# Performance work log

Measured on AMD Instinct MI355X. Metric: run time of the kernel, lower is better.

Reference implementation:

```python
import jax, jax.numpy as jnp
import numpy as np

NEG_INF = -1e9  # 'close_to_negative_inf' constant from the original code


def setup_inputs() -> dict:
    B, S, H, DH, W = 4, 2048, 16, 64, 4
    D = H * DH
    KC = (S - W) // W + 1  # compressed k/v length (VALID conv, stride=W)
    key = jax.random.key(0)
    ks = jax.random.split(key, 9)
    return {
        "pre_q": jax.random.normal(ks[0], (B, S, H, DH), jnp.float32),
        "pre_v": jax.random.normal(ks[1], (B, S, H, DH), jnp.float32),
        "pre_k": jax.random.normal(ks[2], (B, S, H, DH), jnp.float32),
        "output_weights": jax.random.normal(ks[3], (D, D), jnp.float32) * (1.0 / np.sqrt(D)),
        "k_conv_kernel": jax.random.normal(ks[4], (W, DH, DH), jnp.float32) * (1.0 / np.sqrt(W * DH)),
        "k_conv_bias": jnp.zeros((DH,), jnp.float32),
        "v_conv_kernel": jax.random.normal(ks[5], (W, DH, DH), jnp.float32) * (1.0 / np.sqrt(W * DH)),
        "v_conv_bias": jnp.zeros((DH,), jnp.float32),
        "attn_mask": jax.random.randint(ks[6], (B, S, KC), 0, 2, jnp.int32),
    }


def _compress(x, kernel, bias, window):
    # x: (B, H, S, dh) -> conv1d channels_last, stride=window, VALID -> (B, H, Kc, dh)
    B, H, S, dh = x.shape
    x3 = x.reshape(B * H, S, dh)
    y = jax.lax.conv_general_dilated(
        x3, kernel, window_strides=(window,), padding='VALID',
        dimension_numbers=('NWC', 'WIO', 'NWC')) + bias
    return y.reshape(B, H, -1, dh)


def reference(pre_q, pre_v, pre_k, output_weights,
              k_conv_kernel, k_conv_bias, v_conv_kernel, v_conv_bias,
              attn_mask):
    B, Sq, H, dh = pre_q.shape
    d_model = H * dh
    window = k_conv_kernel.shape[0]

    q = jnp.transpose(pre_q, (0, 2, 1, 3))  # (B,H,Sq,dh)
    v = jnp.transpose(pre_v, (0, 2, 1, 3))
    k = jnp.transpose(pre_k, (0, 2, 1, 3))

    # memory-compressed attention: strided conv1d over k and v sequences
    k = _compress(k, k_conv_kernel, k_conv_bias, window)  # (B,H,Kc,dh)
    v = _compress(v, v_conv_kernel, v_conv_bias, window)  # (B,H,Kc,dh)
    Kc = k.shape[2]

    sqrt_d = jnp.sqrt(jnp.float32(d_model // H))

    # batch_dot over merged (B*H) batch dim, exactly as the Keras code
    scores = jnp.matmul(q.reshape(B * H, Sq, dh),
                        jnp.transpose(k, (0, 1, 3, 2)).reshape(B * H, dh, Kc)) / sqrt_d

    # mask_attention: reshape (B*H,q,k) -> (H,B,q,k), apply mask, permute back (faithful to original)
    s4 = scores.reshape(H, B, Sq, Kc)
    m = attn_mask.astype(jnp.float32)  # (B,Sq,Kc), broadcasts over heads
    s4 = s4 * m + (1.0 - m) * NEG_INF
    scores = jnp.transpose(s4, (1, 0, 2, 3)).reshape(B * H, Sq, Kc)

    probs = jax.nn.softmax(scores, axis=-1)  # dropout=0.0 -> identity

    heads = jnp.matmul(probs, v.reshape(B * H, Kc, dh)).reshape(B, H, Sq, dh)
    merged = jnp.transpose(heads, (0, 2, 1, 3)).reshape(-1, d_model)  # (B*Sq, D)
    out = jnp.dot(merged, output_weights).reshape(B, Sq, d_model)
    return out
```

## Files before the change

### kernel.cpp

```cpp
#include <hip/hip_runtime.h>
#include <hip/hip_bf16.h>


typedef __attribute__((ext_vector_type(8))) short short8;
typedef __attribute__((ext_vector_type(4))) short short4v;
typedef __attribute__((ext_vector_type(4))) float f32x4;
typedef __attribute__((ext_vector_type(4))) int int4e;
typedef __attribute__((ext_vector_type(2))) unsigned int u32x2;

#define MFMA32(A, Bf, C) __builtin_amdgcn_mfma_f32_16x16x32_bf16((A), (Bf), (C), 0, 0, 0)
#define MFMA16(A, Bf, C) __builtin_amdgcn_mfma_f32_16x16x16bf16_1k((A), (Bf), (C), 0, 0, 0)

static __device__ __forceinline__ unsigned short f2bf(float f) {
  unsigned int u = __builtin_bit_cast(unsigned int, f);
  u += 0x7fffu + ((u >> 16) & 1u);
  return (unsigned short)(u >> 16);
}
static __device__ __forceinline__ unsigned int pack2c(float a, float b) {
  unsigned short lo = __builtin_bit_cast(unsigned short, __float2bfloat16(a));
  unsigned short hi = __builtin_bit_cast(unsigned short, __float2bfloat16(b));
  return (unsigned int)lo | ((unsigned int)hi << 16);
}
static __device__ __forceinline__ short4v pk4(float a, float b, float c, float d) {
  u32x2 t;
  t[0] = pack2c(a, b);
  t[1] = pack2c(c, d);
  return __builtin_bit_cast(short4v, t);
}
static __device__ __forceinline__ short8 cvt8(f32x4 lo, f32x4 hi) {
  short8 r;
  r[0] = (short)f2bf(lo[0]); r[1] = (short)f2bf(lo[1]);
  r[2] = (short)f2bf(lo[2]); r[3] = (short)f2bf(lo[3]);
  r[4] = (short)f2bf(hi[0]); r[5] = (short)f2bf(hi[1]);
  r[6] = (short)f2bf(hi[2]); r[7] = (short)f2bf(hi[3]);
  return r;
}
static __device__ __forceinline__ short8 cvt8s(f32x4 lo, f32x4 hi, float s) {
  short8 r;
  r[0] = (short)f2bf(lo[0]*s); r[1] = (short)f2bf(lo[1]*s);
  r[2] = (short)f2bf(lo[2]*s); r[3] = (short)f2bf(lo[3]*s);
  r[4] = (short)f2bf(hi[0]*s); r[5] = (short)f2bf(hi[1]*s);
  r[6] = (short)f2bf(hi[2]*s); r[7] = (short)f2bf(hi[3]*s);
  return r;
}
static __device__ __forceinline__ void gl_lds16(const void* g, void* l) {
  __builtin_amdgcn_global_load_lds(
      (const __attribute__((address_space(1))) unsigned int*)g,
      (__attribute__((address_space(3))) unsigned int*)l, 16, 0, 0);
}

__global__ __launch_bounds__(256) void prep_kernel(
    const float* __restrict__ W, unsigned short* __restrict__ WT,
    const float* __restrict__ kck, unsigned short* __restrict__ kkT,
    const float* __restrict__ vck, unsigned short* __restrict__ vkT,
    const int* __restrict__ msk, unsigned int* __restrict__ mpk) {
  __shared__ unsigned short t[64][72];
  const int bid = blockIdx.x;
  const int tid = threadIdx.x;
  if (bid < 256) {
    const int k0 = (bid & 15) * 64, n0 = (bid >> 4) * 64;
    const int cr = tid >> 4, cc = (tid & 15) * 4;
    #pragma unroll
    for (int it = 0; it < 4; ++it) {
      const int kk = it * 16 + cr;
      const f32x4 v = *(const f32x4*)(W + (size_t)(k0 + kk) * 1024 + n0 + cc);
      #pragma unroll
      for (int j = 0; j < 4; ++j) t[cc + j][kk] = f2bf(v[j]);
    }
    __syncthreads();
    const int rn = tid >> 2, seg = tid & 3;
    const short8 w0 = *(const short8*)(&t[rn][seg * 16]);
    const short8 w1 = *(const short8*)(&t[rn][seg * 16 + 8]);
    unsigned short* op = WT + (size_t)(n0 + rn) * 1024 + k0 + seg * 16;
    *(short8*)op = w0;
    *(short8*)(op + 8) = w1;
  } else if (bid < 384) {
    const int tb = bid - 256;
    const float* K = (tb < 64) ? kck : vck;
    unsigned short* KT = (tb < 64) ? kkT : vkT;
    const int idx = (tb & 63) * 256 + tid;
    const int kk = idx >> 6, o = idx & 63;
    KT[o * 256 + kk] = f2bf(K[idx]);
  } else {
    const int w = (bid - 384) * 256 + tid;
    const int* p = msk + (size_t)w * 32;
    unsigned int b = 0;
    #pragma unroll
    for (int i = 0; i < 8; ++i) {
      const int4e v = *(const int4e*)(p + i * 4);
      b |= (unsigned int)(v[0] & 1) << (i * 4);
      b |= (unsigned int)(v[1] & 1) << (i * 4 + 1);
      b |= (unsigned int)(v[2] & 1) << (i * 4 + 2);
      b |= (unsigned int)(v[3] & 1) << (i * 4 + 3);
    }
    mpk[w] = b;
  }
}

__global__ __launch_bounds__(256) void compress_kernel(
    const float* __restrict__ srcK, const unsigned short* __restrict__ kTK,
    const float* __restrict__ biasK, unsigned short* __restrict__ dstK,
    const float* __restrict__ srcV, const unsigned short* __restrict__ kTV,
    const float* __restrict__ biasV, unsigned short* __restrict__ dstV) {
  __shared__ unsigned short t[64 * 72];
  const int bid = blockIdx.x;
  const int tpose = bid >> 9;
  const float* src = tpose ? srcV : srcK;
  const unsigned short* kT = tpose ? kTV : kTK;
  const float* bias = tpose ? biasV : biasK;
  unsigned short* dst = tpose ? dstV : dstK;
  const int tid = threadIdx.x;
  const int wid = tid >> 6, lane = tid & 63;
  const int q = lane & 15, g = lane >> 4;
  const int blockR0 = (bid & 511) * 64;
  const int R0 = blockR0 + wid * 16;
  const int row = R0 + q;
  const int bh = row >> 9, c = row & 511;
  const int b = bh >> 4, h = bh & 15;
  const float* sb = src + (((size_t)b * 2048 + (size_t)c * 4) * 16 + h) * 64;
  f32x4 acc[4];
  #pragma unroll
  for (int ct = 0; ct < 4; ++ct) acc[ct] = f32x4{0.f, 0.f, 0.f, 0.f};
  #pragma unroll
  for (int ch = 0; ch < 8; ++ch) {
    const int kk = ch * 32 + g * 8;
    const int w = kk >> 6, i = kk & 63;
    const float* s8 = sb + (size_t)w * 1024 + i;
    short8 a = cvt8(*(const f32x4*)s8, *(const f32x4*)(s8 + 4));
    #pragma unroll
    for (int ct = 0; ct < 4; ++ct) {
      short8 bf = *(const short8*)(kT + (ct * 16 + q) * 256 + ch * 32 + g * 8);
      acc[ct] = MFMA32(a, bf, acc[ct]);
    }
  }
  #pragma unroll
  for (int ct = 0; ct < 4; ++ct) {
    const int col = ct * 16 + q;
    const float bv = bias[col];
    #pragma unroll
    for (int r = 0; r < 4; ++r) {
      const int lr = wid * 16 + 4 * g + r;
      const unsigned short val = f2bf(acc[ct][r] + bv);
      t[tpose ? (col * 72 + lr) : (lr * 72 + col)] = val;
    }
  }
  __syncthreads();
  const int d = tid >> 2, sq = tid & 3;
  const short8 w0 = *(const short8*)(&t[d * 72 + sq * 16]);
  const short8 w1 = *(const short8*)(&t[d * 72 + sq * 16 + 8]);
  unsigned short* op;
  if (tpose) {
    const int bhb = blockR0 >> 9, cb = blockR0 & 511;
    op = dst + (size_t)bhb * 32768 + (size_t)d * 512 + cb + sq * 16;
  } else {
    op = dst + (size_t)(blockR0 + d) * 64 + sq * 16;
  }
  *(short8*)op = w0;
  *(short8*)(op + 8) = w1;
}

__global__ __launch_bounds__(256) void attn_kernel(
    const float* __restrict__ preq, const unsigned int* __restrict__ mpk,
    const unsigned short* __restrict__ kc, const unsigned short* __restrict__ vt,
    unsigned short* __restrict__ merged) {
  __shared__ unsigned short shm[9728];
  unsigned short* Kl = shm;
  unsigned short* Vl = shm + 4608;
  const int tid = threadIdx.x;
  const int wid = tid >> 6, lane = tid & 63;
  const int q = lane & 15, g = lane >> 4;
  const int bid = blockIdx.x;
  const int x = bid & 7, ii = bid >> 3;
  const int bp = x >> 1;
  const int hp = ((x & 1) << 3) | (ii & 7);
  const int tile = ii >> 3;
  const int jj = hp * 4 + bp;
  const int bin = jj >> 4, hin = jj & 15;
  const int s0 = tile * 128 + wid * 32;

  const float QS = 0.18033688f;
  const float* qpA = preq + (((size_t)bin * 2048 + s0 + q) * 16 + hin) * 64;
  const float* qpB = qpA + 16 * 1024;
  const short8 bqA0 = cvt8s(*(const f32x4*)(qpA + g * 8), *(const f32x4*)(qpA + g * 8 + 4), QS);
  const short8 bqA1 = cvt8s(*(const f32x4*)(qpA + 32 + g * 8), *(const f32x4*)(qpA + 32 + g * 8 + 4), QS);
  const short8 bqB0 = cvt8s(*(const f32x4*)(qpB + g * 8), *(const f32x4*)(qpB + g * 8 + 4), QS);
  const short8 bqB1 = cvt8s(*(const f32x4*)(qpB + 32 + g * 8), *(const f32x4*)(qpB + 32 + g * 8 + 4), QS);

  const unsigned short* kcb = kc + (size_t)jj * 512 * 64;
  const unsigned short* vtb = vt + (size_t)(bp * 16 + hp) * 64 * 512;
  const unsigned int* mrowA = mpk + ((size_t)bp * 2048 + s0 + q) * 16;
  const unsigned int* mrowB = mrowA + 256;

  const int krow = tid >> 3, kc8 = tid & 7;
  const unsigned short* gK = kcb + (size_t)krow * 64 + kc8 * 8;
  unsigned short* lK = Kl + krow * 72 + kc8 * 8;
  const int vrow = tid >> 2, vc4 = tid & 3;
  const unsigned short* gV = vtb + (size_t)vrow * 512 + vc4 * 8;
  unsigned short* lV = Vl + vrow * 40 + vc4 * 8;

  const short4v one4 = {(short)0x3F80, (short)0x3F80, (short)0x3F80, (short)0x3F80};

  f32x4 oA[4], oB[4];
  #pragma unroll
  for (int o = 0; o < 4; ++o) { oA[o] = f32x4{0,0,0,0}; oB[o] = f32x4{0,0,0,0}; }
  f32x4 oSA = {0,0,0,0}, oSB = {0,0,0,0};

  {
    const short8 sK = *(const short8*)gK;
    const short8 sV = *(const short8*)gV;
    *(short8*)lK = sK;
    *(short8*)lV = sV;
  }
  unsigned int mA = mrowA[0], mB = mrowB[0];
  __syncthreads();

  #pragma unroll 2
  for (int c = 0; c < 16; ++c) {
    short8 nK, nV;
    unsigned int nmA = 0, nmB = 0;
    if (c < 15) {
      nK = *(const short8*)(gK + (size_t)(c + 1) * 2048);
      nV = *(const short8*)(gV + (c + 1) * 32);
      nmA = mrowA[c + 1];
      nmB = mrowB[c + 1];
    }
    const unsigned short* Kc_ = Kl + (c & 1) * (32 * 72);
    const unsigned short* Vc_ = Vl + (c & 1) * (64 * 40);
    const short8 ka0 = *(const short8*)(Kc_ + q * 72 + g * 8);
    const short8 ka1 = *(const short8*)(Kc_ + q * 72 + 32 + g * 8);
    const short8 kb0 = *(const short8*)(Kc_ + (16 + q) * 72 + g * 8);
    const short8 kb1 = *(const short8*)(Kc_ + (16 + q) * 72 + 32 + g * 8);
    short4v vf[4][2];
    #pragma unroll
    for (int o = 0; o < 4; ++o) {
      vf[o][0] = *(const short4v*)(Vc_ + (o * 16 + q) * 40 + g * 4);
      vf[o][1] = *(const short4v*)(Vc_ + (o * 16 + q) * 40 + 16 + g * 4);
    }
    __builtin_amdgcn_s_setprio(1);
    f32x4 s0A = {0,0,0,0}; s0A = MFMA32(ka0, bqA0, s0A); s0A = MFMA32(ka1, bqA1, s0A);
    f32x4 s1A = {0,0,0,0}; s1A = MFMA32(kb0, bqA0, s1A); s1A = MFMA32(kb1, bqA1, s1A);
    f32x4 s0B = {0,0,0,0}; s0B = MFMA32(ka0, bqB0, s0B); s0B = MFMA32(ka1, bqB1, s0B);
    f32x4 s1B = {0,0,0,0}; s1B = MFMA32(kb0, bqB0, s1B); s1B = MFMA32(kb1, bqB1, s1B);
    float pA[8], pB[8];
    #pragma unroll
    for (int r = 0; r < 4; ++r) {
      const int b0 = 4 * g + r, b1 = 16 + 4 * g + r;
      pA[r]     = ((mA >> b0) & 1u) ? __builtin_amdgcn_exp2f(s0A[r]) : 0.0f;
      pA[4 + r] = ((mA >> b1) & 1u) ? __builtin_amdgcn_exp2f(s1A[r]) : 0.0f;
      pB[r]     = ((mB >> b0) & 1u) ? __builtin_amdgcn_exp2f(s0B[r]) : 0.0f;
      pB[4 + r] = ((mB >> b1) & 1u) ? __builtin_amdgcn_exp2f(s1B[r]) : 0.0f;
    }
    const short4v pA0 = pk4(pA[0], pA[1], pA[2], pA[3]);
    const short4v pA1 = pk4(pA[4], pA[5], pA[6], pA[7]);
    const short4v pB0 = pk4(pB[0], pB[1], pB[2], pB[3]);
    const short4v pB1 = pk4(pB[4], pB[5], pB[6], pB[7]);
    #pragma unroll
    for (int o = 0; o < 4; ++o) {
      oA[o] = MFMA16(vf[o][0], pA0, oA[o]);
      oA[o] = MFMA16(vf[o][1], pA1, oA[o]);
      oB[o] = MFMA16(vf[o][0], pB0, oB[o]);
      oB[o] = MFMA16(vf[o][1], pB1, oB[o]);
    }
    oSA = MFMA16(one4, pA0, oSA); oSA = MFMA16(one4, pA1, oSA);
    oSB = MFMA16(one4, pB0, oSB); oSB = MFMA16(one4, pB1, oSB);
    __builtin_amdgcn_s_setprio(0);
    if (c < 15) {
      *(short8*)(lK + ((c + 1) & 1) * (32 * 72)) = nK;
      *(short8*)(lV + ((c + 1) & 1) * (64 * 40)) = nV;
    }
    __syncthreads();
    mA = nmA; mB = nmB;
  }

  const float rlA = 1.0f / oSA[0], rlB = 1.0f / oSB[0];

  unsigned short* eb = shm + wid * 2304;
  #pragma unroll
  for (int qs = 0; qs < 2; ++qs) {
    unsigned int* U = (unsigned int*)(eb + qs * 1152);
    const float rl = qs ? rlB : rlA;
    #pragma unroll
    for (int o = 0; o < 4; ++o) {
      const f32x4 ov = qs ? oB[o] : oA[o];
      U[q * 36 + o * 8 + 2 * g]     = pack2c(ov[0] * rl, ov[1] * rl);
      U[q * 36 + o * 8 + 2 * g + 1] = pack2c(ov[2] * rl, ov[3] * rl);
    }
  }
  const int ir = lane >> 2, sg2 = lane & 3;
  #pragma unroll
  for (int qs = 0; qs < 2; ++qs) {
    const unsigned short* ep = eb + qs * 1152;
    const short8 w0 = *(const short8*)(ep + ir * 72 + sg2 * 16);
    const short8 w1 = *(const short8*)(ep + ir * 72 + sg2 * 16 + 8);
    unsigned short* mp = merged + ((size_t)(bp * 2048 + s0 + qs * 16 + ir)) * 1024 + hp * 64 + sg2 * 16;
    *(short8*)mp = w0;
    *(short8*)(mp + 8) = w1;
  }
}

__global__ __launch_bounds__(256) void gemm_kernel(
    const unsigned short* __restrict__ A, const unsigned short* __restrict__ BT,
    float* __restrict__ out) {
  __shared__ unsigned short Bb[4][4096];
  const int tid = threadIdx.x;
  const int wid = tid >> 6, lane = tid & 63;
  const int q = lane & 15, g = lane >> 4;
  const int bid = blockIdx.x;
  const int x = bid & 7, i = bid >> 3;
  const int N0 = (i & 7) * 128;
  const int M0 = (x * 8 + (i >> 3)) * 128 + wid * 32;

  const int r0 = wid * 32 + (lane >> 2);
  const int r1 = r0 + 16;
  const int sc = (lane & 3) * 16;
  const int b0 = sc ^ (((r0 >> 2) & 3) << 4);
  const int b1 = sc ^ (((r1 >> 2) & 3) << 4);
  const unsigned short* gs0 = BT + (size_t)(N0 + r0) * 1024 + (b0 >> 1);
  const unsigned short* gs1 = BT + (size_t)(N0 + r1) * 1024 + (b1 >> 1);
  const int bsz = ((q >> 2) & 3) << 4;

  f32x4 acc[2][8];
  #pragma unroll
  for (int rt = 0; rt < 2; ++rt)
    #pragma unroll
    for (int ct = 0; ct < 8; ++ct) acc[rt][ct] = f32x4{0.f, 0.f, 0.f, 0.f};
  const unsigned short* a0p = A + (size_t)(M0 + q) * 1024 + g * 8;
  const unsigned short* a1p = a0p + 16 * 1024;

  gl_lds16(gs0,      &Bb[0][wid * 1024]);
  gl_lds16(gs1,      &Bb[0][wid * 1024 + 512]);
  gl_lds16(gs0 + 32, &Bb[1][wid * 1024]);
  gl_lds16(gs1 + 32, &Bb[1][wid * 1024 + 512]);
  short8 aC00 = *(const short8*)(a0p);
  short8 aC01 = *(const short8*)(a1p);
  short8 aC10 = *(const short8*)(a0p + 32);
  short8 aC11 = *(const short8*)(a1p + 32);
  __syncthreads();

  for (int t = 0; t < 32; t += 2) {
    if (t < 30) {
      gl_lds16(gs0 + (t + 2) * 32, &Bb[(t + 2) & 3][wid * 1024]);
      gl_lds16(gs1 + (t + 2) * 32, &Bb[(t + 2) & 3][wid * 1024 + 512]);
      gl_lds16(gs0 + (t + 3) * 32, &Bb[(t + 3) & 3][wid * 1024]);
      gl_lds16(gs1 + (t + 3) * 32, &Bb[(t + 3) & 3][wid * 1024 + 512]);
    }
    short8 aN00 = aC00, aN01 = aC01, aN10 = aC10, aN11 = aC11;
    if (t < 30) {
      aN00 = *(const short8*)(a0p + (t + 2) * 32);
      aN01 = *(const short8*)(a1p + (t + 2) * 32);
      aN10 = *(const short8*)(a0p + (t + 3) * 32);
      aN11 = *(const short8*)(a1p + (t + 3) * 32);
    }
    const unsigned short* Bc0 = &Bb[t & 3][0];
    const unsigned short* Bc1 = &Bb[(t + 1) & 3][0];
    #pragma unroll
    for (int ct = 0; ct < 8; ++ct) {
      const int off = (ct * 16 + q) * 32 + (((g * 16) ^ bsz) >> 1);
      const short8 bfr0 = *(const short8*)(Bc0 + off);
      acc[0][ct] = MFMA32(aC00, bfr0, acc[0][ct]);
      acc[1][ct] = MFMA32(aC01, bfr0, acc[1][ct]);
      const short8 bfr1 = *(const short8*)(Bc1 + off);
      acc[0][ct] = MFMA32(aC10, bfr1, acc[0][ct]);
      acc[1][ct] = MFMA32(aC11, bfr1, acc[1][ct]);
    }
    aC00 = aN00; aC01 = aN01; aC10 = aN10; aC11 = aN11;
    __syncthreads();
  }
  #pragma unroll
  for (int rt = 0; rt < 2; ++rt)
    #pragma unroll
    for (int ct = 0; ct < 8; ++ct)
      #pragma unroll
      for (int r = 0; r < 4; ++r)
        out[(size_t)(M0 + rt * 16 + 4 * g + r) * 1024 + N0 + ct * 16 + q] = acc[rt][ct][r];
}

extern "C" void kernel_launch(void* const* d_in, const int* in_sizes, int n_in,
                              void* d_out, int out_size, void* d_ws, size_t ws_size,
                              hipStream_t stream) {
  const float* preq = (const float*)d_in[0];
  const float* prev = (const float*)d_in[1];
  const float* prek = (const float*)d_in[2];
  const float* W    = (const float*)d_in[3];
  const float* kck  = (const float*)d_in[4];
  const float* kcb  = (const float*)d_in[5];
  const float* vck  = (const float*)d_in[6];
  const float* vcb  = (const float*)d_in[7];
  const int*   msk  = (const int*)d_in[8];
  float* out = (float*)d_out;

  char* ws = (char*)d_ws;
  unsigned short* WT  = (unsigned short*)(ws);
  unsigned short* kkT = (unsigned short*)(ws + 2097152);
  unsigned short* vkT = (unsigned short*)(ws + 2129920);
  unsigned short* kcB = (unsigned short*)(ws + 2162688);
  unsigned short* vcT = (unsigned short*)(ws + 6356992);
  unsigned short* mrg = (unsigned short*)(ws + 10551296);
  unsigned int*   mpk = (unsigned int*)(ws + 27328512);

  hipLaunchKernelGGL(prep_kernel, dim3(896), dim3(256), 0, stream,
                     W, WT, kck, kkT, vck, vkT, msk, mpk);
  hipLaunchKernelGGL(compress_kernel, dim3(1024), dim3(256), 0, stream,
                     prek, kkT, kcb, kcB, prev, vkT, vcb, vcT);
  hipLaunchKernelGGL(attn_kernel, dim3(1024), dim3(256), 0, stream, preq, mpk, kcB, vcT, mrg);
  hipLaunchKernelGGL(gemm_kernel, dim3(512), dim3(256), 0, stream, mrg, WT, out);
}
```

Before: 106.0 us.

## Fuse prep and compress kernels; widen attention K/V tiles to 64

Merges the weight/mask prep kernel and the conv-compress kernel into one launch. Each compress block now converts and transposes the raw conv kernel into LDS itself instead of reading a pre-transposed global copy, which removes one launch and one dependency. The attention main loop now processes 64 compressed keys per iteration instead of 32, halving the number of barriers and iterations, with larger double-buffered LDS tiles. The cost is redundant per-block conversion of the conv kernel, more shared memory per block that may lower occupancy, and higher register pressure from holding four P fragments.

```diff
diff --git a/kernel.cpp b/kernel.cpp
--- a/kernel.cpp
+++ b/kernel.cpp
@@ -49,40 +49,105 @@
       (__attribute__((address_space(3))) unsigned int*)l, 16, 0, 0);
 }
 
-__global__ __launch_bounds__(256) void prep_kernel(
+__global__ __launch_bounds__(256) void pre_kernel(
+    const float* __restrict__ srcK, const float* __restrict__ kckRaw,
+    const float* __restrict__ biasK, unsigned short* __restrict__ dstK,
+    const float* __restrict__ srcV, const float* __restrict__ vckRaw,
+    const float* __restrict__ biasV, unsigned short* __restrict__ dstV,
     const float* __restrict__ W, unsigned short* __restrict__ WT,
-    const float* __restrict__ kck, unsigned short* __restrict__ kkT,
-    const float* __restrict__ vck, unsigned short* __restrict__ vkT,
     const int* __restrict__ msk, unsigned int* __restrict__ mpk) {
-  __shared__ unsigned short t[64][72];
+  __shared__ unsigned short shm[21504];
   const int bid = blockIdx.x;
   const int tid = threadIdx.x;
-  if (bid < 256) {
-    const int k0 = (bid & 15) * 64, n0 = (bid >> 4) * 64;
+  if (bid < 1024) {
+    const int tpose = bid >> 9;
+    const float* src = tpose ? srcV : srcK;
+    const float* kraw = tpose ? vckRaw : kckRaw;
+    const float* bias = tpose ? biasV : biasK;
+    unsigned short* dst = tpose ? dstV : dstK;
+    unsigned short* kTl = shm;
+    unsigned short* t = shm + 16896;
+    {
+      const int o = tid & 63, m0 = tid >> 6;
+      #pragma unroll
+      for (int it = 0; it < 8; ++it) {
+        const int kk0 = (it * 4 + m0) * 8;
+        short8 v;
+        #pragma unroll
+        for (int s = 0; s < 8; ++s)
+          v[s] = (short)f2bf(kraw[(size_t)(kk0 + s) * 64 + o]);
+        *(short8*)(kTl + o * 264 + kk0) = v;
+      }
+    }
+    __syncthreads();
+    const int wid = tid >> 6, lane = tid & 63;
+    const int q = lane & 15, g = lane >> 4;
+    const int blockR0 = (bid & 511) * 64;
+    const int R0 = blockR0 + wid * 16;
+    const int row = R0 + q;
+    const int bh = row >> 9, c = row & 511;
+    const int b = bh >> 4, h = bh & 15;
+    const float* sb = src + (((size_t)b * 2048 + (size_t)c * 4) * 16 + h) * 64;
+    f32x4 acc[4];
+    #pragma unroll
+    for (int ct = 0; ct < 4; ++ct) acc[ct] = f32x4{0.f, 0.f, 0.f, 0.f};
+    #pragma unroll
+    for (int ch = 0; ch < 8; ++ch) {
+      const int kk = ch * 32 + g * 8;
+      const int w = kk >> 6, i = kk & 63;
+      const float* s8 = sb + (size_t)w * 1024 + i;
+      short8 a = cvt8(*(const f32x4*)s8, *(const f32x4*)(s8 + 4));
+      #pragma unroll
+      for (int ct = 0; ct < 4; ++ct) {
+        short8 bf = *(const short8*)(kTl + (ct * 16 + q) * 264 + ch * 32 + g * 8);
+        acc[ct] = MFMA32(a, bf, acc[ct]);
+      }
+    }
+    #pragma unroll
+    for (int ct = 0; ct < 4; ++ct) {
+      const int col = ct * 16 + q;
+      const float bv = bias[col];
+      #pragma unroll
+      for (int r = 0; r < 4; ++r) {
+        const int lr = wid * 16 + 4 * g + r;
+        const unsigned short val = f2bf(acc[ct][r] + bv);
+        t[tpose ? (col * 72 + lr) : (lr * 72 + col)] = val;
+      }
+    }
+    __syncthreads();
+    const int d = tid >> 2, sq = tid & 3;
+    const short8 w0 = *(const short8*)(&t[d * 72 + sq * 16]);
+    const short8 w1 = *(const short8*)(&t[d * 72 + sq * 16 + 8]);
+    unsigned short* op;
+    if (tpose) {
+      const int bhb = blockR0 >> 9, cb = blockR0 & 511;
+      op = dst + (size_t)bhb * 32768 + (size_t)d * 512 + cb + sq * 16;
+    } else {
+      op = dst + (size_t)(blockR0 + d) * 64 + sq * 16;
+    }
+    *(short8*)op = w0;
+    *(short8*)(op + 8) = w1;
+  } else if (bid < 1280) {
+    unsigned short (*t2)[72] = (unsigned short (*)[72])shm;
+    const int wb = bid - 1024;
+    const int k0 = (wb & 15) * 64, n0 = (wb >> 4) * 64;
     const int cr = tid >> 4, cc = (tid & 15) * 4;
     #pragma unroll
     for (int it = 0; it < 4; ++it) {
       const int kk = it * 16 + cr;
       const f32x4 v = *(const f32x4*)(W + (size_t)(k0 + kk) * 1024 + n0 + cc);
       #pragma unroll
-      for (int j = 0; j < 4; ++j) t[cc + j][kk] = f2bf(v[j]);
+      for (int j = 0; j < 4; ++j) t2[cc + j][kk] = f2bf(v[j]);
     }
     __syncthreads();
     const int rn = tid >> 2, seg = tid & 3;
-    const short8 w0 = *(const short8*)(&t[rn][seg * 16]);
-    const short8 w1 = *(const short8*)(&t[rn][seg * 16 + 8]);
+    const short8 w0 = *(const short8*)(&t2[rn][seg * 16]);
+    const short8 w1 = *(const short8*)(&t2[rn][seg * 16 + 8]);
     unsigned short* op = WT + (size_t)(n0 + rn) * 1024 + k0 + seg * 16;
     *(short8*)op = w0;
     *(short8*)(op + 8) = w1;
-  } else if (bid < 384) {
-    const int tb = bid - 256;
-    const float* K = (tb < 64) ? kck : vck;
-    unsigned short* KT = (tb < 64) ? kkT : vkT;
-    const int idx = (tb & 63) * 256 + tid;
-    const int kk = idx >> 6, o = idx & 63;
-    KT[o * 256 + kk] = f2bf(K[idx]);
   } else {
-    const int w = (bid - 384) * 256 + tid;
+    const int w = (bid - 1280) * 256 + tid;
     const int* p = msk + (size_t)w * 32;
     unsigned int b = 0;
     #pragma unroll
@@ -97,75 +162,13 @@
   }
 }
 
-__global__ __launch_bounds__(256) void compress_kernel(
-    const float* __restrict__ srcK, const unsigned short* __restrict__ kTK,
-    const float* __restrict__ biasK, unsigned short* __restrict__ dstK,
-    const float* __restrict__ srcV, const unsigned short* __restrict__ kTV,
-    const float* __restrict__ biasV, unsigned short* __restrict__ dstV) {
-  __shared__ unsigned short t[64 * 72];
-  const int bid = blockIdx.x;
-  const int tpose = bid >> 9;
-  const float* src = tpose ? srcV : srcK;
-  const unsigned short* kT = tpose ? kTV : kTK;
-  const float* bias = tpose ? biasV : biasK;
-  unsigned short* dst = tpose ? dstV : dstK;
-  const int tid = threadIdx.x;
-  const int wid = tid >> 6, lane = tid & 63;
-  const int q = lane & 15, g = lane >> 4;
-  const int blockR0 = (bid & 511) * 64;
-  const int R0 = blockR0 + wid * 16;
-  const int row = R0 + q;
-  const int bh = row >> 9, c = row & 511;
-  const int b = bh >> 4, h = bh & 15;
-  const float* sb = src + (((size_t)b * 2048 + (size_t)c * 4) * 16 + h) * 64;
-  f32x4 acc[4];
-  #pragma unroll
-  for (int ct = 0; ct < 4; ++ct) acc[ct] = f32x4{0.f, 0.f, 0.f, 0.f};
-  #pragma unroll
-  for (int ch = 0; ch < 8; ++ch) {
-    const int kk = ch * 32 + g * 8;
-    const int w = kk >> 6, i = kk & 63;
-    const float* s8 = sb + (size_t)w * 1024 + i;
-    short8 a = cvt8(*(const f32x4*)s8, *(const f32x4*)(s8 + 4));
-    #pragma unroll
-    for (int ct = 0; ct < 4; ++ct) {
-      short8 bf = *(const short8*)(kT + (ct * 16 + q) * 256 + ch * 32 + g * 8);
-      acc[ct] = MFMA32(a, bf, acc[ct]);
-    }
-  }
-  #pragma unroll
-  for (int ct = 0; ct < 4; ++ct) {
-    const int col = ct * 16 + q;
-    const float bv = bias[col];
-    #pragma unroll
-    for (int r = 0; r < 4; ++r) {
-      const int lr = wid * 16 + 4 * g + r;
-      const unsigned short val = f2bf(acc[ct][r] + bv);
-      t[tpose ? (col * 72 + lr) : (lr * 72 + col)] = val;
-    }
-  }
-  __syncthreads();
-  const int d = tid >> 2, sq = tid & 3;
-  const short8 w0 = *(const short8*)(&t[d * 72 + sq * 16]);
-  const short8 w1 = *(const short8*)(&t[d * 72 + sq * 16 + 8]);
-  unsigned short* op;
-  if (tpose) {
-    const int bhb = blockR0 >> 9, cb = blockR0 & 511;
-    op = dst + (size_t)bhb * 32768 + (size_t)d * 512 + cb + sq * 16;
-  } else {
-    op = dst + (size_t)(blockR0 + d) * 64 + sq * 16;
-  }
-  *(short8*)op = w0;
-  *(short8*)(op + 8) = w1;
-}
-
 __global__ __launch_bounds__(256) void attn_kernel(
     const float* __restrict__ preq, const unsigned int* __restrict__ mpk,
     const unsigned short* __restrict__ kc, const unsigned short* __restrict__ vt,
     unsigned short* __restrict__ merged) {
-  __shared__ unsigned short shm[9728];
+  __shared__ unsigned short shm[18432];
   unsigned short* Kl = shm;
-  unsigned short* Vl = shm + 4608;
+  unsigned short* Vl = shm + 9216;
   const int tid = threadIdx.x;
   const int wid = tid >> 6, lane = tid & 63;
   const int q = lane & 15, g = lane >> 4;
@@ -191,12 +194,15 @@
   const unsigned int* mrowA = mpk + ((size_t)bp * 2048 + s0 + q) * 16;
   const unsigned int* mrowB = mrowA + 256;
 
-  const int krow = tid >> 3, kc8 = tid & 7;
-  const unsigned short* gK = kcb + (size_t)krow * 64 + kc8 * 8;
-  unsigned short* lK = Kl + krow * 72 + kc8 * 8;
-  const int vrow = tid >> 2, vc4 = tid & 3;
-  const unsigned short* gV = vtb + (size_t)vrow * 512 + vc4 * 8;
-  unsigned short* lV = Vl + vrow * 40 + vc4 * 8;
+  const int sr = tid >> 3, sseg = tid & 7;
+  const unsigned short* gK0 = kcb + (size_t)sr * 64 + sseg * 8;
+  const unsigned short* gK1 = gK0 + 32 * 64;
+  unsigned short* lK0 = Kl + sr * 72 + sseg * 8;
+  unsigned short* lK1 = lK0 + 32 * 72;
+  const unsigned short* gV0 = vtb + (size_t)sr * 512 + sseg * 8;
+  const unsigned short* gV1 = gV0 + 32 * 512;
+  unsigned short* lV0 = Vl + sr * 72 + sseg * 8;
+  unsigned short* lV1 = lV0 + 32 * 72;
 
   const short4v one4 = {(short)0x3F80, (short)0x3F80, (short)0x3F80, (short)0x3F80};
 
@@ -205,71 +211,71 @@
   for (int o = 0; o < 4; ++o) { oA[o] = f32x4{0,0,0,0}; oB[o] = f32x4{0,0,0,0}; }
   f32x4 oSA = {0,0,0,0}, oSB = {0,0,0,0};
 
-  {
-    const short8 sK = *(const short8*)gK;
-    const short8 sV = *(const short8*)gV;
-    *(short8*)lK = sK;
-    *(short8*)lV = sV;
-  }
-  unsigned int mA = mrowA[0], mB = mrowB[0];
+  *(short8*)lK0 = *(const short8*)gK0;
+  *(short8*)lK1 = *(const short8*)gK1;
+  *(short8*)lV0 = *(const short8*)gV0;
+  *(short8*)lV1 = *(const short8*)gV1;
+  u32x2 mA2 = *(const u32x2*)mrowA;
+  u32x2 mB2 = *(const u32x2*)mrowB;
   __syncthreads();
 
   #pragma unroll 2
-  for (int c = 0; c < 16; ++c) {
-    short8 nK, nV;
-    unsigned int nmA = 0, nmB = 0;
-    if (c < 15) {
-      nK = *(const short8*)(gK + (size_t)(c + 1) * 2048);
-      nV = *(const short8*)(gV + (c + 1) * 32);
-      nmA = mrowA[c + 1];
-      nmB = mrowB[c + 1];
-    }
-    const unsigned short* Kc_ = Kl + (c & 1) * (32 * 72);
-    const unsigned short* Vc_ = Vl + (c & 1) * (64 * 40);
-    const short8 ka0 = *(const short8*)(Kc_ + q * 72 + g * 8);
-    const short8 ka1 = *(const short8*)(Kc_ + q * 72 + 32 + g * 8);
-    const short8 kb0 = *(const short8*)(Kc_ + (16 + q) * 72 + g * 8);
-    const short8 kb1 = *(const short8*)(Kc_ + (16 + q) * 72 + 32 + g * 8);
-    short4v vf[4][2];
+  for (int sc = 0; sc < 8; ++sc) {
+    short8 nK0, nK1, nV0, nV1;
+    u32x2 nmA = {0, 0}, nmB = {0, 0};
+    if (sc < 7) {
+      nK0 = *(const short8*)(gK0 + (size_t)(sc + 1) * 4096);
+      nK1 = *(const short8*)(gK1 + (size_t)(sc + 1) * 4096);
+      nV0 = *(const short8*)(gV0 + (sc + 1) * 64);
+      nV1 = *(const short8*)(gV1 + (sc + 1) * 64);
+      nmA = *(const u32x2*)(mrowA + 2 * (sc + 1));
+      nmB = *(const u32x2*)(mrowB + 2 * (sc + 1));
+    }
+    const unsigned short* Kc_ = Kl + (sc & 1) * 4608;
+    const unsigned short* Vc_ = Vl + (sc & 1) * 4608;
+    __builtin_amdgcn_s_setprio(1);
+    short4v pA[4], pB[4];
+    #pragma unroll
+    for (int sub = 0; sub < 4; ++sub) {
+      const short8 k0 = *(const short8*)(Kc_ + (sub * 16 + q) * 72 + g * 8);
+      const short8 k1 = *(const short8*)(Kc_ + (sub * 16 + q) * 72 + 32 + g * 8);
+      f32x4 sA = {0,0,0,0}; sA = MFMA32(k0, bqA0, sA); sA = MFMA32(k1, bqA1, sA);
+      f32x4 sB = {0,0,0,0}; sB = MFMA32(k0, bqB0, sB); sB = MFMA32(k1, bqB1, sB);
+      const unsigned int wA = mA2[sub >> 1], wB = mB2[sub >> 1];
+      const int bb = (sub & 1) * 16 + 4 * g;
+      float eA[4], eB[4];
+      #pragma unroll
+      for (int r = 0; r < 4; ++r) {
+        eA[r] = ((wA >> (bb + r)) & 1u) ? __builtin_amdgcn_exp2f(sA[r]) : 0.0f;
+        eB[r] = ((wB >> (bb + r)) & 1u) ? __builtin_amdgcn_exp2f(sB[r]) : 0.0f;
+      }
+      pA[sub] = pk4(eA[0], eA[1], eA[2], eA[3]);
+      pB[sub] = pk4(eB[0], eB[1], eB[2], eB[3]);
+    }
     #pragma unroll
     for (int o = 0; o < 4; ++o) {
-      vf[o][0] = *(const short4v*)(Vc_ + (o * 16 + q) * 40 + g * 4);
-      vf[o][1] = *(const short4v*)(Vc_ + (o * 16 + q) * 40 + 16 + g * 4);
-    }
-    __builtin_amdgcn_s_setprio(1);
-    f32x4 s0A = {0,0,0,0}; s0A = MFMA32(ka0, bqA0, s0A); s0A = MFMA32(ka1, bqA1, s0A);
-    f32x4 s1A = {0,0,0,0}; s1A = MFMA32(kb0, bqA0, s1A); s1A = MFMA32(kb1, bqA1, s1A);
-    f32x4 s0B = {0,0,0,0}; s0B = MFMA32(ka0, bqB0, s0B); s0B = MFMA32(ka1, bqB1, s0B);
-    f32x4 s1B = {0,0,0,0}; s1B = MFMA32(kb0, bqB0, s1B); s1B = MFMA32(kb1, bqB1, s1B);
-    float pA[8], pB[8];
-    #pragma unroll
-    for (int r = 0; r < 4; ++r) {
-      const int b0 = 4 * g + r, b1 = 16 + 4 * g + r;
-      pA[r]     = ((mA >> b0) & 1u) ? __builtin_amdgcn_exp2f(s0A[r]) : 0.0f;
-      pA[4 + r] = ((mA >> b1) & 1u) ? __builtin_amdgcn_exp2f(s1A[r]) : 0.0f;
-      pB[r]     = ((mB >> b0) & 1u) ? __builtin_amdgcn_exp2f(s0B[r]) : 0.0f;
-      pB[4 + r] = ((mB >> b1) & 1u) ? __builtin_amdgcn_exp2f(s1B[r]) : 0.0f;
-    }
-    const short4v pA0 = pk4(pA[0], pA[1], pA[2], pA[3]);
-    const short4v pA1 = pk4(pA[4], pA[5], pA[6], pA[7]);
-    const short4v pB0 = pk4(pB[0], pB[1], pB[2], pB[3]);
-    const short4v pB1 = pk4(pB[4], pB[5], pB[6], pB[7]);
-    #pragma unroll
-    for (int o = 0; o < 4; ++o) {
-      oA[o] = MFMA16(vf[o][0], pA0, oA[o]);
-      oA[o] = MFMA16(vf[o][1], pA1, oA[o]);
-      oB[o] = MFMA16(vf[o][0], pB0, oB[o]);
-      oB[o] = MFMA16(vf[o][1], pB1, oB[o]);
-    }
-    oSA = MFMA16(one4, pA0, oSA); oSA = MFMA16(one4, pA1, oSA);
-    oSB = MFMA16(one4, pB0, oSB); oSB = MFMA16(one4, pB1, oSB);
+      #pragma unroll
+      for (int sub = 0; sub < 4; ++sub) {
+        const short4v vfr = *(const short4v*)(Vc_ + (o * 16 + q) * 72 + sub * 16 + g * 4);
+        oA[o] = MFMA16(vfr, pA[sub], oA[o]);
+        oB[o] = MFMA16(vfr, pB[sub], oB[o]);
+      }
+    }
+    #pragma unroll
+    for (int sub = 0; sub < 4; ++sub) {
+      oSA = MFMA16(one4, pA[sub], oSA);
+      oSB = MFMA16(one4, pB[sub], oSB);
+    }
     __builtin_amdgcn_s_setprio(0);
-    if (c < 15) {
-      *(short8*)(lK + ((c + 1) & 1) * (32 * 72)) = nK;
-      *(short8*)(lV + ((c + 1) & 1) * (64 * 40)) = nV;
+    if (sc < 7) {
+      const int nb = ((sc + 1) & 1) * 4608;
+      *(short8*)(lK0 + nb) = nK0;
+      *(short8*)(lK1 + nb) = nK1;
+      *(short8*)(lV0 + nb) = nV0;
+      *(short8*)(lV1 + nb) = nV1;
     }
     __syncthreads();
-    mA = nmA; mB = nmB;
+    mA2 = nmA; mB2 = nmB;
   }
 
   const float rlA = 1.0f / oSA[0], rlB = 1.0f / oSB[0];
@@ -391,17 +397,13 @@
 
   char* ws = (char*)d_ws;
   unsigned short* WT  = (unsigned short*)(ws);
-  unsigned short* kkT = (unsigned short*)(ws + 2097152);
-  unsigned short* vkT = (unsigned short*)(ws + 2129920);
   unsigned short* kcB = (unsigned short*)(ws + 2162688);
   unsigned short* vcT = (unsigned short*)(ws + 6356992);
   unsigned short* mrg = (unsigned short*)(ws + 10551296);
   unsigned int*   mpk = (unsigned int*)(ws + 27328512);
 
-  hipLaunchKernelGGL(prep_kernel, dim3(896), dim3(256), 0, stream,
-                     W, WT, kck, kkT, vck, vkT, msk, mpk);
-  hipLaunchKernelGGL(compress_kernel, dim3(1024), dim3(256), 0, stream,
-                     prek, kkT, kcb, kcB, prev, vkT, vcb, vcT);
+  hipLaunchKernelGGL(pre_kernel, dim3(1792), dim3(256), 0, stream,
+                     prek, kck, kcb, kcB, prev, vck, vcb, vcT, W, WT, msk, mpk);
   hipLaunchKernelGGL(attn_kernel, dim3(1024), dim3(256), 0, stream, preq, mpk, kcB, vcT, mrg);
   hipLaunchKernelGGL(gemm_kernel, dim3(512), dim3(256), 0, stream, mrg, WT, out);
 }
```

Measured after the change: 91.26 us. 13.9% less time.
